# Optimization experiments

Hardware: AMD Instinct MI355X
Metric: run time of the kernel (lower is better)

The kernel has to match this reference:

```python
import jax, jax.numpy as jnp
import numpy as np

B, L, E, H = 2, 256, 512, 8
HD = E // H  # 64


def setup_inputs() -> dict:
    key = jax.random.key(0)
    ks = jax.random.split(key, 11)
    w_scale = 0.04  # ~ xavier std for 512x512
    return {
        "query": jax.random.normal(ks[0], (B, L, E), jnp.float32),
        "key": jax.random.normal(ks[1], (B, L, E), jnp.float32),
        "value": jax.random.normal(ks[2], (B, L, E), jnp.float32),
        "relation": jax.random.normal(ks[3], (B, L, L, E), jnp.float32),
        "Wq": jax.random.normal(ks[4], (E, E), jnp.float32) * w_scale,
        "Wk": jax.random.normal(ks[5], (E, E), jnp.float32) * w_scale,
        "Wv": jax.random.normal(ks[6], (E, E), jnp.float32) * w_scale,
        "Wr": jax.random.normal(ks[7], (E, E), jnp.float32) * w_scale,
        "br": jnp.zeros((E,), jnp.float32),
        "Wo": jax.random.normal(ks[8], (E, E), jnp.float32) * w_scale,
        "bo": jnp.zeros((E,), jnp.float32),
    }


def reference(query, key, value, relation, Wq, Wk, Wv, Wr, br, Wo, bo):
    # relation_project: nn.Linear -> x @ W.T + b, (B,L,L,E)
    r = relation @ Wr.T + br
    # source uses right-multiplication by raw parameter matrices,
    # and (faithfully) projects value with the QUERY weight.
    q = query @ Wq    # (B,L,E)
    k = key @ Wk      # (B,L,E)
    v = value @ Wq    # bug preserved from source
    q = q.reshape(B, L, H, HD)
    k = k.reshape(B, L, H, HD)
    v = v.reshape(B, L, H, HD)
    # q broadcast over key positions plus per-pair relation bias: (B,L,L,H,HD)
    qr = q[:, :, None, :, :] + r.reshape(B, L, L, H, HD)
    a = jnp.einsum('bqkhe,bkhe->bqkh', qr, k) / jnp.sqrt(jnp.float32(HD))
    a = jax.nn.softmax(a, axis=2)  # softmax over key positions (dim 2)
    attn = jnp.einsum('bqkh,bkhe->bqhe', a, v).reshape(B, L, E)
    out = attn @ Wo.T + bo  # out_proj
    return out, a
```

## Files before the change

### kernel.cpp

```cpp
#include <hip/hip_runtime.h>

#define DEV_INLINE __device__ __forceinline__

typedef float nfloat4 __attribute__((ext_vector_type(4)));

static constexpr int Bb = 2, Ls = 256, E = 512, H = 8;
static constexpr int BL = Bb * Ls;

static constexpr size_t WS_QP = 0;
static constexpr size_t WS_KP = WS_QP + (size_t)BL * E;
static constexpr size_t WS_VP = WS_KP + (size_t)BL * E;
static constexpr size_t WS_M  = WS_VP + (size_t)BL * E;
static constexpr size_t WS_C  = WS_M  + (size_t)BL * H * E;
static constexpr size_t WS_O  = WS_C  + (size_t)BL * H;
static constexpr size_t WS_QK = WS_O  + (size_t)BL * E;

DEV_INLINE float dot4n(nfloat4 a, float4 b) {
  return a.x * b.x + a.y * b.y + a.z * b.z + a.w * b.w;
}

template <int TRANSB>
DEV_INLINE void gemm_tile(const float* __restrict__ A, int lda,
                          const float* __restrict__ B, int ldb,
                          float* __restrict__ C, int ldc, int Ksz,
                          const float* __restrict__ bias) {
  __shared__ float As[16][68];
  __shared__ float Bs[16][68];
  const int t = threadIdx.x;
  const int tx = t & 15, ty = t >> 4;
  const int ar = t >> 2, ac = t & 3;
  const int i0 = blockIdx.y * 64, j0 = blockIdx.x * 64;
  float acc[4][4] = {};
  for (int k0 = 0; k0 < Ksz; k0 += 16) {
    {
      float4 av = *(const float4*)&A[(size_t)(i0 + ar) * lda + (k0 + 4 * ac)];
      As[4 * ac + 0][ar] = av.x;
      As[4 * ac + 1][ar] = av.y;
      As[4 * ac + 2][ar] = av.z;
      As[4 * ac + 3][ar] = av.w;
    }
    if (TRANSB == 0) {
      float4 bv = *(const float4*)&B[(size_t)(k0 + ty) * ldb + (j0 + 4 * tx)];
      *(float4*)&Bs[ty][4 * tx] = bv;
    } else {
      float4 bv = *(const float4*)&B[(size_t)(j0 + ar) * ldb + (k0 + 4 * ac)];
      Bs[4 * ac + 0][ar] = bv.x;
      Bs[4 * ac + 1][ar] = bv.y;
      Bs[4 * ac + 2][ar] = bv.z;
      Bs[4 * ac + 3][ar] = bv.w;
    }
    __syncthreads();
#pragma unroll
    for (int kk = 0; kk < 16; ++kk) {
      float4 a4 = *(const float4*)&As[kk][ty * 4];
      float4 b4 = *(const float4*)&Bs[kk][tx * 4];
      acc[0][0] += a4.x * b4.x; acc[0][1] += a4.x * b4.y;
      acc[0][2] += a4.x * b4.z; acc[0][3] += a4.x * b4.w;
      acc[1][0] += a4.y * b4.x; acc[1][1] += a4.y * b4.y;
      acc[1][2] += a4.y * b4.z; acc[1][3] += a4.y * b4.w;
      acc[2][0] += a4.z * b4.x; acc[2][1] += a4.z * b4.y;
      acc[2][2] += a4.z * b4.z; acc[2][3] += a4.z * b4.w;
      acc[3][0] += a4.w * b4.x; acc[3][1] += a4.w * b4.y;
      acc[3][2] += a4.w * b4.z; acc[3][3] += a4.w * b4.w;
    }
    __syncthreads();
  }
#pragma unroll
  for (int r = 0; r < 4; ++r) {
#pragma unroll
    for (int c2 = 0; c2 < 4; ++c2) {
      float v = acc[r][c2];
      if (bias) v += bias[j0 + tx * 4 + c2];
      C[(size_t)(i0 + ty * 4 + r) * ldc + (j0 + tx * 4 + c2)] = v;
    }
  }
}

__global__ __launch_bounds__(256) void k1_proj(
    const float* __restrict__ q, const float* __restrict__ k,
    const float* __restrict__ v, const float* __restrict__ Wq,
    const float* __restrict__ Wk, float* __restrict__ qp,
    float* __restrict__ kp, float* __restrict__ vp) {
  const float* A; const float* Bm; float* C;
  switch (blockIdx.z) {
    case 0:  A = q; Bm = Wq; C = qp; break;
    case 1:  A = k; Bm = Wk; C = kp; break;
    default: A = v; Bm = Wq; C = vp; break;
  }
  gemm_tile<0>(A, 512, Bm, 512, C, 512, 512, nullptr);
}

__global__ __launch_bounds__(256) void k2_M(const float* __restrict__ kp,
                                            const float* __restrict__ Wr,
                                            const float* __restrict__ br,
                                            float* __restrict__ M,
                                            float* __restrict__ c) {
  const int h = blockIdx.z;
  if (blockIdx.x == 0 && threadIdx.x < 64) {
    const int row = blockIdx.y * 64 + threadIdx.x;
    float s = 0.f;
    const float* kr = kp + (size_t)row * 512 + h * 64;
    const float* bb = br + h * 64;
#pragma unroll 8
    for (int d = 0; d < 64; ++d) s += bb[d] * kr[d];
    c[((size_t)(row >> 8) * 8 + h) * 256 + (row & 255)] = s;
  }
  gemm_tile<0>(kp + h * 64, 512, Wr + (size_t)h * 64 * 512, 512,
               M + (size_t)h * 512, 4096, 64, nullptr);
}

__global__ __launch_bounds__(256) void k3_qk(const float* __restrict__ qp,
                                             const float* __restrict__ kp,
                                             const float* __restrict__ c,
                                             float* __restrict__ qk) {
  const int z = blockIdx.z;
  const int b = z >> 3, h = z & 7;
  gemm_tile<1>(qp + (size_t)b * 256 * 512 + h * 64, 512,
               kp + (size_t)b * 256 * 512 + h * 64, 512,
               qk + (size_t)z * 65536, 256, 64,
               c + (size_t)z * 256);
}

__global__ __launch_bounds__(256) void k4_rel(
    const float* __restrict__ rel, const float* __restrict__ Mw,
    const float* __restrict__ qk, float* __restrict__ logits) {
  const int blk = blockIdx.x;
  const int bk = blk >> 2;
  const int qq = blk & 3;
  const int b = bk >> 8, k = bk & 255;
  const int t = threadIdx.x, w = t >> 6, lane = t & 63;

  const float* Mbase = Mw + (size_t)bk * 8 * 512;
  float4 m0[8], m1[8];
#pragma unroll
  for (int h = 0; h < 8; ++h) {
    m0[h] = *(const float4*)(Mbase + h * 512 + 4 * lane);
    m1[h] = *(const float4*)(Mbase + h * 512 + 256 + 4 * lane);
  }

  const int hw = ((lane & 1) << 2) | (lane & 2) | ((lane >> 2) & 1);

  const int q0 = qq * 64 + w;
  const nfloat4* relp =
      (const nfloat4*)(rel) + (((size_t)b * 256 + q0) * 256 + k) * 128;
  const float* qkp = qk + ((size_t)(b * 8 + hw) * 256 + q0) * 256 + k;
  float* lp = logits + (((size_t)b * 256 + q0) * 256 + k) * 8 + hw;
  const bool writer = (lane < 8);
  const size_t REL_STRIDE = (size_t)4 * 256 * 128;
  const size_t QK_STRIDE = (size_t)4 * 256;
  const size_t L_STRIDE = (size_t)4 * 256 * 8;

  const bool b0 = (lane & 1) != 0;
  const bool b1 = (lane & 2) != 0;
  const bool b2 = (lane & 4) != 0;

  nfloat4 r0 = __builtin_nontemporal_load(&relp[lane]);
  nfloat4 r1 = __builtin_nontemporal_load(&relp[64 + lane]);

  for (int i = 0; i < 16; ++i) {
    float qkv = 0.f;
    if (writer) qkv = *qkp;

    const bool more = (i < 15);
    nfloat4 nr0, nr1;
    if (more) {
      relp += REL_STRIDE;
      nr0 = __builtin_nontemporal_load(&relp[lane]);
      nr1 = __builtin_nontemporal_load(&relp[64 + lane]);
    }

    float acc[8];
#pragma unroll
    for (int h = 0; h < 8; ++h)
      acc[h] = dot4n(r0, m0[h]) + dot4n(r1, m1[h]);

    float s[4];
#pragma unroll
    for (int j = 0; j < 4; ++j) {
      float lo = acc[j], hi = acc[j + 4];
      float send = b0 ? lo : hi;
      float keep = b0 ? hi : lo;
      s[j] = keep + __shfl_xor(send, 1);
    }
    float u[2];
#pragma unroll
    for (int j = 0; j < 2; ++j) {
      float lo = s[j], hi = s[j + 2];
      float send = b1 ? lo : hi;
      float keep = b1 ? hi : lo;
      u[j] = keep + __shfl_xor(send, 2);
    }
    {
      float lo = u[0], hi = u[1];
      float send = b2 ? lo : hi;
      float keep = b2 ? hi : lo;
      float v = keep + __shfl_xor(send, 4);
      v += __shfl_xor(v, 8);
      v += __shfl_xor(v, 16);
      v += __shfl_xor(v, 32);
      if (writer) *lp = v + qkv;
    }
    if (more) { r0 = nr0; r1 = nr1; }
    qkp += QK_STRIDE;
    lp += L_STRIDE;
  }
}

__global__ __launch_bounds__(256) void k5_softmax(float* __restrict__ logits,
                                                  const float* __restrict__ vp,
                                                  float* __restrict__ o) {
  const int bq = blockIdx.x;
  const int b = bq >> 8;
  const int t = threadIdx.x;
  float* L = logits + (size_t)bq * 2048;
  float4 x0 = ((float4*)L)[t * 2];
  float4 x1 = ((float4*)L)[t * 2 + 1];
  float x[8] = {x0.x, x0.y, x0.z, x0.w, x1.x, x1.y, x1.z, x1.w};
  const float SCALE = 0.125f;
#pragma unroll
  for (int j = 0; j < 8; ++j) x[j] *= SCALE;

  __shared__ float tr[8][272];
  __shared__ float mx[8], sm[8];
  __shared__ float ob[512];
#pragma unroll
  for (int hh = 0; hh < 8; ++hh) tr[hh][t] = x[hh];
  __syncthreads();
  const int g = t >> 5, j = t & 31;
  float m = -1e30f;
#pragma unroll
  for (int i = 0; i < 8; ++i) m = fmaxf(m, tr[g][j + 32 * i]);
#pragma unroll
  for (int off = 16; off >= 1; off >>= 1) m = fmaxf(m, __shfl_down(m, off, 32));
  if (j == 0) mx[g] = m;
  __syncthreads();
  float p[8];
#pragma unroll
  for (int hh = 0; hh < 8; ++hh) p[hh] = __expf(x[hh] - mx[hh]);
#pragma unroll
  for (int hh = 0; hh < 8; ++hh) tr[hh][t] = p[hh];
  __syncthreads();
  float ss = 0.f;
#pragma unroll
  for (int i = 0; i < 8; ++i) ss += tr[g][j + 32 * i];
#pragma unroll
  for (int off = 16; off >= 1; off >>= 1) ss += __shfl_down(ss, off, 32);
  if (j == 0) sm[g] = ss;
  __syncthreads();
  float inv[8];
#pragma unroll
  for (int hh = 0; hh < 8; ++hh) inv[hh] = 1.0f / sm[hh];
#pragma unroll
  for (int hh = 0; hh < 8; ++hh) x[hh] = p[hh] * inv[hh];
  ((float4*)L)[t * 2] = make_float4(x[0], x[1], x[2], x[3]);
  ((float4*)L)[t * 2 + 1] = make_float4(x[4], x[5], x[6], x[7]);

  const int g2 = t >> 7, tc = t & 127;
  const int hc = tc >> 4;
  const float invh = inv[hc];
  const float4* V4 =
      (const float4*)(vp + (size_t)b * 256 * 512 + (size_t)g2 * 128 * 512) + tc;
  const float* trh = &tr[hc][g2 * 128];
  float ax = 0.f, ay = 0.f, az = 0.f, aw = 0.f;
#pragma unroll 8
  for (int kk = 0; kk < 128; ++kk) {
    const float wgt = trh[kk];
    float4 vv = V4[(size_t)kk * 128];
    ax += wgt * vv.x;
    ay += wgt * vv.y;
    az += wgt * vv.z;
    aw += wgt * vv.w;
  }
  if (g2) {
    ob[4 * tc + 0] = ax;
    ob[4 * tc + 1] = ay;
    ob[4 * tc + 2] = az;
    ob[4 * tc + 3] = aw;
  }
  __syncthreads();
  if (!g2) {
    ax = (ax + ob[4 * tc + 0]) * invh;
    ay = (ay + ob[4 * tc + 1]) * invh;
    az = (az + ob[4 * tc + 2]) * invh;
    aw = (aw + ob[4 * tc + 3]) * invh;
    ((float4*)(o + (size_t)bq * 512))[tc] = make_float4(ax, ay, az, aw);
  }
}

__global__ __launch_bounds__(256) void k6_out(const float* __restrict__ o,
                                              const float* __restrict__ Wo,
                                              const float* __restrict__ bo,
                                              float* __restrict__ out) {
  gemm_tile<1>(o, 512, Wo, 512, out, 512, 512, bo);
}

extern "C" void kernel_launch(void* const* d_in, const int* in_sizes, int n_in,
                              void* d_out, int out_size, void* d_ws,
                              size_t ws_size, hipStream_t stream) {
  const float* query = (const float*)d_in[0];
  const float* key   = (const float*)d_in[1];
  const float* value = (const float*)d_in[2];
  const float* rel   = (const float*)d_in[3];
  const float* Wq    = (const float*)d_in[4];
  const float* Wk    = (const float*)d_in[5];
  const float* Wr    = (const float*)d_in[7];
  const float* br    = (const float*)d_in[8];
  const float* Wo    = (const float*)d_in[9];
  const float* bo    = (const float*)d_in[10];

  float* out = (float*)d_out;
  float* a   = (float*)d_out + (size_t)BL * E;

  float* ws = (float*)d_ws;
  float* qp  = ws + WS_QP;
  float* kp  = ws + WS_KP;
  float* vp  = ws + WS_VP;
  float* M   = ws + WS_M;
  float* c   = ws + WS_C;
  float* o   = ws + WS_O;
  float* qkb = ws + WS_QK;

  k1_proj<<<dim3(8, 8, 3), 256, 0, stream>>>(query, key, value, Wq, Wk, qp, kp, vp);
  k2_M<<<dim3(8, 8, 8), 256, 0, stream>>>(kp, Wr, br, M, c);
  k3_qk<<<dim3(4, 4, 16), 256, 0, stream>>>(qp, kp, c, qkb);
  k4_rel<<<dim3(2048), 256, 0, stream>>>(rel, M, qkb, a);
  k5_softmax<<<dim3(512), 256, 0, stream>>>(a, vp, o);
  k6_out<<<dim3(8, 8, 1), 256, 0, stream>>>(o, Wo, bo, out);
}
```

Baseline: 462.8 us.

## Merge M and QK kernels, prefetch GEMM tiles, retile GEMMs, pair softmax rows

Merges the M-projection and QK GEMM launches into one kernel, moving the per-key bias c into the relation-logit kernel so the two no longer depend on each other. The shared GEMM tile now register-prefetches the next K slice and takes a template rows-per-thread parameter, used to launch more, smaller blocks for the projection and output GEMMs. The softmax kernel handles two query rows per block so each V load serves both rows. Together these aim to cut launch count and raise occupancy on the small GEMMs, at the cost of more register pressure and fewer softmax blocks.

After: 437.5 us, median of 2. 1.06x faster.

```diff
diff --git a/kernel.cpp b/kernel.cpp
--- a/kernel.cpp
+++ b/kernel.cpp
@@ -19,59 +19,81 @@
   return a.x * b.x + a.y * b.y + a.z * b.z + a.w * b.w;
 }
 
-template <int TRANSB>
+template <int TRANSB, int RPT>
 DEV_INLINE void gemm_tile(const float* __restrict__ A, int lda,
                           const float* __restrict__ B, int ldb,
                           float* __restrict__ C, int ldc, int Ksz,
-                          const float* __restrict__ bias) {
-  __shared__ float As[16][68];
+                          const float* __restrict__ bias, int i0, int j0) {
+  constexpr int TM = 16 * RPT;
+  __shared__ float As[16][TM + 4];
   __shared__ float Bs[16][68];
   const int t = threadIdx.x;
   const int tx = t & 15, ty = t >> 4;
   const int ar = t >> 2, ac = t & 3;
-  const int i0 = blockIdx.y * 64, j0 = blockIdx.x * 64;
-  float acc[4][4] = {};
+  const bool aload = (t < 64 * RPT);
+  float acc[RPT][4] = {};
+
+  float4 av, bv;
+  if (aload) av = *(const float4*)&A[(size_t)(i0 + ar) * lda + 4 * ac];
+  if (TRANSB == 0)
+    bv = *(const float4*)&B[(size_t)ty * ldb + (j0 + 4 * tx)];
+  else
+    bv = *(const float4*)&B[(size_t)(j0 + ar) * ldb + 4 * ac];
+
   for (int k0 = 0; k0 < Ksz; k0 += 16) {
-    {
-      float4 av = *(const float4*)&A[(size_t)(i0 + ar) * lda + (k0 + 4 * ac)];
+    if (aload) {
       As[4 * ac + 0][ar] = av.x;
       As[4 * ac + 1][ar] = av.y;
       As[4 * ac + 2][ar] = av.z;
       As[4 * ac + 3][ar] = av.w;
     }
     if (TRANSB == 0) {
-      float4 bv = *(const float4*)&B[(size_t)(k0 + ty) * ldb + (j0 + 4 * tx)];
       *(float4*)&Bs[ty][4 * tx] = bv;
     } else {
-      float4 bv = *(const float4*)&B[(size_t)(j0 + ar) * ldb + (k0 + 4 * ac)];
       Bs[4 * ac + 0][ar] = bv.x;
       Bs[4 * ac + 1][ar] = bv.y;
       Bs[4 * ac + 2][ar] = bv.z;
       Bs[4 * ac + 3][ar] = bv.w;
     }
     __syncthreads();
+    const int k1 = k0 + 16;
+    if (k1 < Ksz) {
+      if (aload) av = *(const float4*)&A[(size_t)(i0 + ar) * lda + (k1 + 4 * ac)];
+      if (TRANSB == 0)
+        bv = *(const float4*)&B[(size_t)(k1 + ty) * ldb + (j0 + 4 * tx)];
+      else
+        bv = *(const float4*)&B[(size_t)(j0 + ar) * ldb + (k1 + 4 * ac)];
+    }
 #pragma unroll
     for (int kk = 0; kk < 16; ++kk) {
-      float4 a4 = *(const float4*)&As[kk][ty * 4];
+      float a[RPT];
+      if constexpr (RPT == 4) {
+        float4 a4 = *(const float4*)&As[kk][ty * 4];
+        a[0] = a4.x; a[1] = a4.y; a[2] = a4.z; a[3] = a4.w;
+      } else if constexpr (RPT == 2) {
+        float2 a2 = *(const float2*)&As[kk][ty * 2];
+        a[0] = a2.x; a[1] = a2.y;
+      } else {
+        a[0] = As[kk][ty];
+      }
       float4 b4 = *(const float4*)&Bs[kk][tx * 4];
-      acc[0][0] += a4.x * b4.x; acc[0][1] += a4.x * b4.y;
-      acc[0][2] += a4.x * b4.z; acc[0][3] += a4.x * b4.w;
-      acc[1][0] += a4.y * b4.x; acc[1][1] += a4.y * b4.y;
-      acc[1][2] += a4.y * b4.z; acc[1][3] += a4.y * b4.w;
-      acc[2][0] += a4.z * b4.x; acc[2][1] += a4.z * b4.y;
-      acc[2][2] += a4.z * b4.z; acc[2][3] += a4.z * b4.w;
-      acc[3][0] += a4.w * b4.x; acc[3][1] += a4.w * b4.y;
-      acc[3][2] += a4.w * b4.z; acc[3][3] += a4.w * b4.w;
+#pragma unroll
+      for (int r = 0; r < RPT; ++r) {
+        acc[r][0] += a[r] * b4.x;
+        acc[r][1] += a[r] * b4.y;
+        acc[r][2] += a[r] * b4.z;
+        acc[r][3] += a[r] * b4.w;
+      }
     }
     __syncthreads();
   }
 #pragma unroll
-  for (int r = 0; r < 4; ++r) {
+  for (int r = 0; r < RPT; ++r) {
 #pragma unroll
     for (int c2 = 0; c2 < 4; ++c2) {
       float v = acc[r][c2];
       if (bias) v += bias[j0 + tx * 4 + c2];
-      C[(size_t)(i0 + ty * 4 + r) * ldc + (j0 + tx * 4 + c2)] = v;
+      C[(size_t)(i0 + ty * RPT + r) * ldc + (j0 + tx * 4 + c2)] = v;
     }
   }
 }
@@ -87,43 +109,44 @@
     case 1:  A = k; Bm = Wk; C = kp; break;
     default: A = v; Bm = Wq; C = vp; break;
   }
-  gemm_tile<0>(A, 512, Bm, 512, C, 512, 512, nullptr);
-}
-
-__global__ __launch_bounds__(256) void k2_M(const float* __restrict__ kp,
-                                            const float* __restrict__ Wr,
-                                            const float* __restrict__ br,
-                                            float* __restrict__ M,
-                                            float* __restrict__ c) {
-  const int h = blockIdx.z;
-  if (blockIdx.x == 0 && threadIdx.x < 64) {
-    const int row = blockIdx.y * 64 + threadIdx.x;
-    float s = 0.f;
-    const float* kr = kp + (size_t)row * 512 + h * 64;
-    const float* bb = br + h * 64;
+  gemm_tile<0, 2>(A, 512, Bm, 512, C, 512, 512, nullptr,
+                  blockIdx.y * 32, blockIdx.x * 64);
+}
+
+__global__ __launch_bounds__(256) void k23(
+    const float* __restrict__ kp, const float* __restrict__ Wr,
+    const float* __restrict__ br, const float* __restrict__ qp,
+    float* __restrict__ M, float* __restrict__ c, float* __restrict__ qk) {
+  const int blk = blockIdx.x;
+  if (blk < 512) {
+    const int h = blk >> 6, rem = blk & 63;
+    const int by = rem >> 3, bx = rem & 7;
+    if (bx == 0 && threadIdx.x < 64) {
+      const int row = by * 64 + threadIdx.x;
+      float s = 0.f;
+      const float* kr = kp + (size_t)row * 512 + h * 64;
+      const float* bb = br + h * 64;
 #pragma unroll 8
-    for (int d = 0; d < 64; ++d) s += bb[d] * kr[d];
-    c[((size_t)(row >> 8) * 8 + h) * 256 + (row & 255)] = s;
-  }
-  gemm_tile<0>(kp + h * 64, 512, Wr + (size_t)h * 64 * 512, 512,
-               M + (size_t)h * 512, 4096, 64, nullptr);
-}
-
-__global__ __launch_bounds__(256) void k3_qk(const float* __restrict__ qp,
-                                             const float* __restrict__ kp,
-                                             const float* __restrict__ c,
-                                             float* __restrict__ qk) {
-  const int z = blockIdx.z;
-  const int b = z >> 3, h = z & 7;
-  gemm_tile<1>(qp + (size_t)b * 256 * 512 + h * 64, 512,
-               kp + (size_t)b * 256 * 512 + h * 64, 512,
-               qk + (size_t)z * 65536, 256, 64,
-               c + (size_t)z * 256);
+      for (int d = 0; d < 64; ++d) s += bb[d] * kr[d];
+      c[((size_t)(row >> 8) * 8 + h) * 256 + (row & 255)] = s;
+    }
+    gemm_tile<0, 4>(kp + h * 64, 512, Wr + (size_t)h * 64 * 512, 512,
+                    M + (size_t)h * 512, 4096, 64, nullptr, by * 64, bx * 64);
+  } else {
+    const int idx = blk - 512;
+    const int z = idx >> 4;
+    const int by = (idx >> 2) & 3, bx = idx & 3;
+    const int b = z >> 3, h = z & 7;
+    gemm_tile<1, 4>(qp + (size_t)b * 256 * 512 + h * 64, 512,
+                    kp + (size_t)b * 256 * 512 + h * 64, 512,
+                    qk + (size_t)z * 65536, 256, 64, nullptr, by * 64, bx * 64);
+  }
 }
 
 __global__ __launch_bounds__(256) void k4_rel(
     const float* __restrict__ rel, const float* __restrict__ Mw,
-    const float* __restrict__ qk, float* __restrict__ logits) {
+    const float* __restrict__ qk, const float* __restrict__ cbias,
+    float* __restrict__ logits) {
   const int blk = blockIdx.x;
   const int bk = blk >> 2;
   const int qq = blk & 3;
@@ -139,13 +162,14 @@
   }
 
   const int hw = ((lane & 1) << 2) | (lane & 2) | ((lane >> 2) & 1);
+  const bool writer = (lane < 8);
+  const float cv = writer ? cbias[((size_t)b * 8 + hw) * 256 + k] : 0.f;
 
   const int q0 = qq * 64 + w;
   const nfloat4* relp =
       (const nfloat4*)(rel) + (((size_t)b * 256 + q0) * 256 + k) * 128;
   const float* qkp = qk + ((size_t)(b * 8 + hw) * 256 + q0) * 256 + k;
   float* lp = logits + (((size_t)b * 256 + q0) * 256 + k) * 8 + hw;
-  const bool writer = (lane < 8);
   const size_t REL_STRIDE = (size_t)4 * 256 * 128;
   const size_t QK_STRIDE = (size_t)4 * 256;
   const size_t L_STRIDE = (size_t)4 * 256 * 8;
@@ -198,7 +222,7 @@
       v += __shfl_xor(v, 8);
       v += __shfl_xor(v, 16);
       v += __shfl_xor(v, 32);
-      if (writer) *lp = v + qkv;
+      if (writer) *lp = v + qkv + cv;
     }
     if (more) { r0 = nr0; r1 = nr1; }
     qkp += QK_STRIDE;
@@ -209,81 +233,107 @@
 __global__ __launch_bounds__(256) void k5_softmax(float* __restrict__ logits,
                                                   const float* __restrict__ vp,
                                                   float* __restrict__ o) {
-  const int bq = blockIdx.x;
-  const int b = bq >> 8;
+  const int pr = blockIdx.x;
+  const int bq0 = pr * 2;
+  const int b = bq0 >> 8;
   const int t = threadIdx.x;
-  float* L = logits + (size_t)bq * 2048;
-  float4 x0 = ((float4*)L)[t * 2];
-  float4 x1 = ((float4*)L)[t * 2 + 1];
-  float x[8] = {x0.x, x0.y, x0.z, x0.w, x1.x, x1.y, x1.z, x1.w};
   const float SCALE = 0.125f;
-#pragma unroll
-  for (int j = 0; j < 8; ++j) x[j] *= SCALE;
-
-  __shared__ float tr[8][272];
-  __shared__ float mx[8], sm[8];
-  __shared__ float ob[512];
-#pragma unroll
-  for (int hh = 0; hh < 8; ++hh) tr[hh][t] = x[hh];
+
+  __shared__ float tr[2][8][272];
+  __shared__ float mx[2][8], sm[2][8];
+  __shared__ float ob[2][512];
+
+  float x[2][8];
+#pragma unroll
+  for (int r = 0; r < 2; ++r) {
+    float* L = logits + (size_t)(bq0 + r) * 2048;
+    float4 x0 = ((float4*)L)[t * 2];
+    float4 x1 = ((float4*)L)[t * 2 + 1];
+    x[r][0] = x0.x; x[r][1] = x0.y; x[r][2] = x0.z; x[r][3] = x0.w;
+    x[r][4] = x1.x; x[r][5] = x1.y; x[r][6] = x1.z; x[r][7] = x1.w;
+#pragma unroll
+    for (int j = 0; j < 8; ++j) x[r][j] *= SCALE;
+#pragma unroll
+    for (int hh = 0; hh < 8; ++hh) tr[r][hh][t] = x[r][hh];
+  }
   __syncthreads();
   const int g = t >> 5, j = t & 31;
-  float m = -1e30f;
-#pragma unroll
-  for (int i = 0; i < 8; ++i) m = fmaxf(m, tr[g][j + 32 * i]);
-#pragma unroll
-  for (int off = 16; off >= 1; off >>= 1) m = fmaxf(m, __shfl_down(m, off, 32));
-  if (j == 0) mx[g] = m;
-  __syncthreads();
-  float p[8];
-#pragma unroll
-  for (int hh = 0; hh < 8; ++hh) p[hh] = __expf(x[hh] - mx[hh]);
-#pragma unroll
-  for (int hh = 0; hh < 8; ++hh) tr[hh][t] = p[hh];
-  __syncthreads();
-  float ss = 0.f;
-#pragma unroll
-  for (int i = 0; i < 8; ++i) ss += tr[g][j + 32 * i];
-#pragma unroll
-  for (int off = 16; off >= 1; off >>= 1) ss += __shfl_down(ss, off, 32);
-  if (j == 0) sm[g] = ss;
-  __syncthreads();
-  float inv[8];
-#pragma unroll
-  for (int hh = 0; hh < 8; ++hh) inv[hh] = 1.0f / sm[hh];
-#pragma unroll
-  for (int hh = 0; hh < 8; ++hh) x[hh] = p[hh] * inv[hh];
-  ((float4*)L)[t * 2] = make_float4(x[0], x[1], x[2], x[3]);
-  ((float4*)L)[t * 2 + 1] = make_float4(x[4], x[5], x[6], x[7]);
+#pragma unroll
+  for (int r = 0; r < 2; ++r) {
+    float m = -1e30f;
+#pragma unroll
+    for (int i = 0; i < 8; ++i) m = fmaxf(m, tr[r][g][j + 32 * i]);
+#pragma unroll
+    for (int off = 16; off >= 1; off >>= 1) m = fmaxf(m, __shfl_down(m, off, 32));
+    if (j == 0) mx[r][g] = m;
+  }
+  __syncthreads();
+  float p[2][8];
+#pragma unroll
+  for (int r = 0; r < 2; ++r)
+#pragma unroll
+    for (int hh = 0; hh < 8; ++hh) p[r][hh] = __expf(x[r][hh] - mx[r][hh]);
+#pragma unroll
+  for (int r = 0; r < 2; ++r)
+#pragma unroll
+    for (int hh = 0; hh < 8; ++hh) tr[r][hh][t] = p[r][hh];
+  __syncthreads();
+#pragma unroll
+  for (int r = 0; r < 2; ++r) {
+    float ss = 0.f;
+#pragma unroll
+    for (int i = 0; i < 8; ++i) ss += tr[r][g][j + 32 * i];
+#pragma unroll
+    for (int off = 16; off >= 1; off >>= 1) ss += __shfl_down(ss, off, 32);
+    if (j == 0) sm[r][g] = ss;
+  }
+  __syncthreads();
+#pragma unroll
+  for (int r = 0; r < 2; ++r) {
+    float inv[8];
+#pragma unroll
+    for (int hh = 0; hh < 8; ++hh) inv[hh] = 1.0f / sm[r][hh];
+    float* L = logits + (size_t)(bq0 + r) * 2048;
+    ((float4*)L)[t * 2] = make_float4(p[r][0] * inv[0], p[r][1] * inv[1],
+                                      p[r][2] * inv[2], p[r][3] * inv[3]);
+    ((float4*)L)[t * 2 + 1] = make_float4(p[r][4] * inv[4], p[r][5] * inv[5],
+                                          p[r][6] * inv[6], p[r][7] * inv[7]);
+  }
 
   const int g2 = t >> 7, tc = t & 127;
   const int hc = tc >> 4;
-  const float invh = inv[hc];
   const float4* V4 =
       (const float4*)(vp + (size_t)b * 256 * 512 + (size_t)g2 * 128 * 512) + tc;
-  const float* trh = &tr[hc][g2 * 128];
-  float ax = 0.f, ay = 0.f, az = 0.f, aw = 0.f;
+  const float* t0 = &tr[0][hc][g2 * 128];
+  const float* t1 = &tr[1][hc][g2 * 128];
+  float a0x = 0.f, a0y = 0.f, a0z = 0.f, a0w = 0.f;
+  float a1x = 0.f, a1y = 0.f, a1z = 0.f, a1w = 0.f;
 #pragma unroll 8
   for (int kk = 0; kk < 128; ++kk) {
-    const float wgt = trh[kk];
     float4 vv = V4[(size_t)kk * 128];
-    ax += wgt * vv.x;
-    ay += wgt * vv.y;
-    az += wgt * vv.z;
-    aw += wgt * vv.w;
+    const float w0 = t0[kk], w1 = t1[kk];
+    a0x += w0 * vv.x; a0y += w0 * vv.y; a0z += w0 * vv.z; a0w += w0 * vv.w;
+    a1x += w1 * vv.x; a1y += w1 * vv.y; a1z += w1 * vv.z; a1w += w1 * vv.w;
   }
   if (g2) {
-    ob[4 * tc + 0] = ax;
-    ob[4 * tc + 1] = ay;
-    ob[4 * tc + 2] = az;
-    ob[4 * tc + 3] = aw;
+    ob[0][4 * tc + 0] = a0x; ob[0][4 * tc + 1] = a0y;
+    ob[0][4 * tc + 2] = a0z; ob[0][4 * tc + 3] = a0w;
+    ob[1][4 * tc + 0] = a1x; ob[1][4 * tc + 1] = a1y;
+    ob[1][4 * tc + 2] = a1z; ob[1][4 * tc + 3] = a1w;
   }
   __syncthreads();
   if (!g2) {
-    ax = (ax + ob[4 * tc + 0]) * invh;
-    ay = (ay + ob[4 * tc + 1]) * invh;
-    az = (az + ob[4 * tc + 2]) * invh;
-    aw = (aw + ob[4 * tc + 3]) * invh;
-    ((float4*)(o + (size_t)bq * 512))[tc] = make_float4(ax, ay, az, aw);
+    const float i0 = 1.0f / sm[0][hc], i1 = 1.0f / sm[1][hc];
+    a0x = (a0x + ob[0][4 * tc + 0]) * i0;
+    a0y = (a0y + ob[0][4 * tc + 1]) * i0;
+    a0z = (a0z + ob[0][4 * tc + 2]) * i0;
+    a0w = (a0w + ob[0][4 * tc + 3]) * i0;
+    a1x = (a1x + ob[1][4 * tc + 0]) * i1;
+    a1y = (a1y + ob[1][4 * tc + 1]) * i1;
+    a1z = (a1z + ob[1][4 * tc + 2]) * i1;
+    a1w = (a1w + ob[1][4 * tc + 3]) * i1;
+    ((float4*)(o + (size_t)bq0 * 512))[tc] = make_float4(a0x, a0y, a0z, a0w);
+    ((float4*)(o + (size_t)(bq0 + 1) * 512))[tc] = make_float4(a1x, a1y, a1z, a1w);
   }
 }
 
@@ -291,7 +341,8 @@
                                               const float* __restrict__ Wo,
                                               const float* __restrict__ bo,
                                               float* __restrict__ out) {
-  gemm_tile<1>(o, 512, Wo, 512, out, 512, 512, bo);
+  gemm_tile<1, 1>(o, 512, Wo, 512, out, 512, 512, bo,
+                  blockIdx.y * 16, blockIdx.x * 64);
 }
 
 extern "C" void kernel_launch(void* const* d_in, const int* in_sizes, int n_in,
@@ -320,10 +371,9 @@
   float* o   = ws + WS_O;
   float* qkb = ws + WS_QK;
 
-  k1_proj<<<dim3(8, 8, 3), 256, 0, stream>>>(query, key, value, Wq, Wk, qp, kp, vp);
-  k2_M<<<dim3(8, 8, 8), 256, 0, stream>>>(kp, Wr, br, M, c);
-  k3_qk<<<dim3(4, 4, 16), 256, 0, stream>>>(qp, kp, c, qkb);
-  k4_rel<<<dim3(2048), 256, 0, stream>>>(rel, M, qkb, a);
-  k5_softmax<<<dim3(512), 256, 0, stream>>>(a, vp, o);
-  k6_out<<<dim3(8, 8, 1), 256, 0, stream>>>(o, Wo, bo, out);
-}
+  k1_proj<<<dim3(8, 16, 3), 256, 0, stream>>>(query, key, value, Wq, Wk, qp, kp, vp);
+  k23<<<dim3(768), 256, 0, stream>>>(kp, Wr, br, qp, M, c, qkb);
+  k4_rel<<<dim3(2048), 256, 0, stream>>>(rel, M, qkb, c, a);
+  k5_softmax<<<dim3(256), 256, 0, stream>>>(a, vp, o);
+  k6_out<<<dim3(8, 32, 1), 256, 0, stream>>>(o, Wo, bo, out);
+}
```
